# Optimization experiments

Measured on AMD Instinct MI355X. Metric: run time of the kernel, lower is better.

The kernel has to match this reference:

```python
import math
import jax, jax.numpy as jnp
import numpy as np

TEMPERATURE = 1.0
TARGET_VARIANCE = 2.0


def _l2_normalize(x, eps=1e-12):
    # matches F.normalize(dim=-1): x / max(||x||_2, eps)
    n = jnp.linalg.norm(x, axis=-1, keepdims=True)
    return x / jnp.maximum(n, eps)


def setup_inputs() -> dict:
    key = jax.random.key(0)
    k1, k2, k3 = jax.random.split(key, 3)
    B, L, D = 16, 2048, 512
    embs = jax.random.normal(k1, (B, L, D), dtype=jnp.float32)
    clip_embs = jax.random.normal(k2, (B, L, D), dtype=jnp.float32)
    mask = jax.random.randint(k3, (B, L), 0, 2, dtype=jnp.int32)
    return {"embs": embs, "clip_embs": clip_embs, "mask": mask}


def reference(embs, clip_embs, mask):
    B, L, D = embs.shape
    p = _l2_normalize(embs)
    q = _l2_normalize(clip_embs)

    # m_b = number of valid tokens per sample; original slices the first m rows
    m = jnp.sum(mask > 0, axis=-1)                      # [B]
    valid = jnp.arange(L)[None, :] < m[:, None]         # [B, L]
    colm = valid[:, None, :]                            # [B, 1, L] column mask

    # batched p @ q^T over the full padded length, masked afterwards
    logits = jnp.einsum('bid,bjd->bij', p, q) / TEMPERATURE  # [B, L, L]
    neg = jnp.finfo(logits.dtype).min
    logp = jax.nn.log_softmax(jnp.where(colm, logits, neg), axis=-1)

    # Gaussian distance weights: base_weight[i, j] = |i - j|
    idx = jnp.arange(L)
    dist = jnp.abs(idx[:, None] - idx[None, :]).astype(embs.dtype)  # [L, L]
    t_un = jnp.exp(-(dist ** 2) / (2.0 * TARGET_VARIANCE ** 2)) / TARGET_VARIANCE * math.sqrt(math.pi * 2.0)
    target = jax.nn.softmax(jnp.where(colm, t_un[None], neg), axis=-1)  # [B, L, L]

    # KL(target || softmax(logits)) = target * (log target - logp), summed over cols
    safe_t = jnp.where(colm, target, 1.0)
    kl = jnp.where(colm, target * (jnp.log(safe_t) - logp), 0.0)
    row_sum = jnp.sum(kl, axis=-1)                      # [B, L]

    # mean over the m valid rows, then mean over batch
    per_sample = jnp.sum(jnp.where(valid, row_sum, 0.0), axis=-1) / m.astype(embs.dtype)
    return jnp.sum(per_sample) / B
```

## Files before the change

kernel.cpp:

```cpp
#include <hip/hip_runtime.h>
#include <hip/hip_bf16.h>

#define BB 16
#define LL 2048
#define DD 512
#define BL (BB*LL)
#define RADIUS 15
#define CF 1.25331414f
#define NSL 6
#define NII 16

typedef __attribute__((ext_vector_type(8))) short short8_t;
typedef __attribute__((ext_vector_type(4))) float f32x4;

static __device__ __forceinline__ unsigned short f2bf(float x){
  unsigned int u = __float_as_uint(x);
  return (unsigned short)((u + 0x7fffu + ((u >> 16) & 1u)) >> 16);
}

static __device__ __forceinline__ void gld_lds16(const void* g, void* l){
  __builtin_amdgcn_global_load_lds(
      (const __attribute__((address_space(1))) unsigned int*)g,
      (__attribute__((address_space(3))) unsigned int*)l, 16, 0, 0);
}

#if __has_builtin(__builtin_amdgcn_cvt_pk_fp8_f32)
static __device__ __forceinline__ long f2fp8x8(float4 x0, float4 x1){
  int w0 = __builtin_amdgcn_cvt_pk_fp8_f32(x0.x, x0.y, 0, false);
  w0     = __builtin_amdgcn_cvt_pk_fp8_f32(x0.z, x0.w, w0, true);
  int w1 = __builtin_amdgcn_cvt_pk_fp8_f32(x1.x, x1.y, 0, false);
  w1     = __builtin_amdgcn_cvt_pk_fp8_f32(x1.z, x1.w, w1, true);
  return ((long)(unsigned)w1 << 32) | (unsigned)w0;
}
#else
static __device__ __forceinline__ unsigned f2fp8_1(float xf){
  unsigned x = __float_as_uint(xf);
  unsigned s = (x >> 24) & 0x80u;
  unsigned ax = x & 0x7fffffffu;
  if (ax >= 0x43e80000u) return s | 0x7eu;
  if (ax <  0x3a800000u) return s;
  unsigned exp = ax >> 23;
  if (exp <= 120){
    unsigned man = (ax & 0x7fffffu) | 0x800000u;
    int rsh = 141 - (int)exp;
    unsigned keep = man >> rsh;
    unsigned rem  = man & ((1u << rsh) - 1u);
    unsigned half = 1u << (rsh - 1);
    keep += (rem > half || (rem == half && (keep & 1u)));
    return s | keep;
  }
  unsigned keep = ax >> 20;
  unsigned rem  = ax & 0xfffffu;
  keep += (rem > 0x80000u || (rem == 0x80000u && (keep & 1u)));
  int code = (int)keep - (120 << 3);
  if (code >= 0x7f) code = 0x7e;
  return s | (unsigned)code;
}
static __device__ __forceinline__ long f2fp8x8(float4 x0, float4 x1){
  unsigned long o = 0;
  o |= (unsigned long)f2fp8_1(x0.x);
  o |= (unsigned long)f2fp8_1(x0.y) << 8;
  o |= (unsigned long)f2fp8_1(x0.z) << 16;
  o |= (unsigned long)f2fp8_1(x0.w) << 24;
  o |= (unsigned long)f2fp8_1(x1.x) << 32;
  o |= (unsigned long)f2fp8_1(x1.y) << 40;
  o |= (unsigned long)f2fp8_1(x1.z) << 48;
  o |= (unsigned long)f2fp8_1(x1.w) << 56;
  return (long)o;
}
#endif


__global__ void mcount_kernel(const int* __restrict__ mask, int* __restrict__ mout){
  int b = blockIdx.x;
  int s = 0;
  for (int j = threadIdx.x; j < LL; j += 256) s += (mask[(size_t)b*LL + j] > 0) ? 1 : 0;
  __shared__ int sred[256];
  sred[threadIdx.x] = s; __syncthreads();
  for (int k = 128; k; k >>= 1){
    if (threadIdx.x < k) sred[threadIdx.x] += sred[threadIdx.x + k];
    __syncthreads();
  }
  if (threadIdx.x == 0) mout[b] = sred[0];
}

__global__ __launch_bounds__(256) void precvt(const float* __restrict__ embs,
                                              const float* __restrict__ clip,
                                              const int* __restrict__ mcnt,
                                              unsigned char* __restrict__ p8,
                                              unsigned char* __restrict__ q8){
  const int lane = threadIdx.x & 63;
  for (int gw = blockIdx.x * 4 + (threadIdx.x >> 6); gw < 2 * BL; gw += 4096 * 4){
    const float* src; unsigned char* dst; int r, b;
    if (gw < BL){ b = gw >> 11; r = gw & 2047; src = embs + (size_t)gw * DD;
                  dst = p8 + (size_t)b * LL * DD; }
    else { int g = gw - BL; b = g >> 11; r = g & 2047; src = clip + (size_t)g * DD;
           dst = q8 + (size_t)b * LL * DD; }
    const int RND = (mcnt[b] + 127) & ~127;
    if (r >= RND) continue;
    float4 x0 = *(const float4*)(src + lane * 8);
    float4 x1 = *(const float4*)(src + lane * 8 + 4);
    float ss = x0.x*x0.x + x0.y*x0.y + x0.z*x0.z + x0.w*x0.w
             + x1.x*x1.x + x1.y*x1.y + x1.z*x1.z + x1.w*x1.w;
    #pragma unroll
    for (int m = 1; m < 64; m <<= 1) ss += __shfl_xor(ss, m, 64);
    float s = 1.0f / fmaxf(sqrtf(ss), 1e-12f);
    float4 y0 = make_float4(x0.x*s, x0.y*s, x0.z*s, x0.w*s);
    float4 y1 = make_float4(x1.x*s, x1.y*s, x1.z*s, x1.w*s);
    long o = f2fp8x8(y0, y1);
    const int kswz = (lane & 3) ^ ((r >> 2) & 3);
    *(long*)(dst + ((size_t)((lane >> 2) * LL + r) << 5) + (kswz << 3)) = o;
  }
}

__global__ __launch_bounds__(256, 4) void gram8(
    const unsigned char* __restrict__ p8, const unsigned char* __restrict__ q8,
    const int* __restrict__ mcnt, float* __restrict__ part )
{
  const int bid = blockIdx.x;
  const int xcd = bid & 7;
  const int b   = (xcd << 1) | ((bid >> 3) & 1);
  const int ii  = (bid >> 4) & (NII - 1);
  const int js  = bid >> 8;
  const int M   = mcnt[b];
  const int nIt = (M + 127) >> 7;
  if (ii >= nIt) return;

  __shared__ alignas(16) unsigned char bsm[3][8192];
  __shared__ float gt[RADIUS + 1];

  const int tid  = threadIdx.x;
  const int wave = tid >> 6;
  const int lane = tid & 63;
  const int col  = lane & 15;
  const int kg   = lane >> 4;
  const int kswz = (kg ^ (col >> 2)) << 3;

  if (tid <= RADIUS)
    gt[tid] = expm1f(CF * __expf(-(float)(tid * tid) * 0.125f));
  __syncthreads();

  const unsigned char* pb = p8 + (size_t)b * LL * DD;
  const unsigned char* qb = q8 + (size_t)b * LL * DD;
  const int njt = (M + 15) >> 4;
  const int S   = (njt > js) ? ((njt - js + NSL - 1) / NSL) : 0;
  if (S == 0) return;

  #define STAGE(BF, JT) do {                                                     \
    const int _j0 = (JT) << 4;                                                   \
    _Pragma("unroll")                                                            \
    for (int u = 0; u < 2; ++u){                                                 \
      const int _kb0 = (wave << 1) + (u << 3);                                   \
      gld_lds16(qb + ((size_t)((_kb0 + (lane >> 5)) * LL + _j0) << 5)            \
                   + ((lane & 31) << 4),                                         \
                (void*)&bsm[BF][_kb0 << 9]);                                     \
    }                                                                            \
  } while (0)

  const int iw = (ii << 7) + (wave << 5);

  long a0[16], a1[16];
  #pragma unroll
  for (int kb = 0; kb < 16; ++kb){
    a0[kb] = *(const long*)(pb + ((size_t)(kb * LL + iw      + col) << 5) + kswz);
    a1[kb] = *(const long*)(pb + ((size_t)(kb * LL + iw + 16 + col) << 5) + kswz);
  }
  #pragma unroll
  for (int kb = 0; kb < 16; ++kb){
    asm volatile("" : "+v"(a0[kb]));
    asm volatile("" : "+v"(a1[kb]));
  }

  float es0[4]={0,0,0,0}, ls0[4]={0,0,0,0}, bg0[4]={0,0,0,0};
  float es1[4]={0,0,0,0}, ls1[4]={0,0,0,0}, bg1[4]={0,0,0,0};

  STAGE(0, js);
  if (S > 1) STAGE(1, js + NSL);

  for (int s = 0; s < S; ++s){
    if (s + 1 < S) { asm volatile("s_waitcnt vmcnt(2)" ::: "memory"); }
    else           { asm volatile("s_waitcnt vmcnt(0)" ::: "memory"); }
    __builtin_amdgcn_s_barrier();
    __builtin_amdgcn_sched_barrier(0);
    if (s + 2 < S) STAGE((s + 2) % 3, js + NSL * (s + 2));

    const int j0 = (js + NSL * s) << 4;
    f32x4 c0 = {0.f,0.f,0.f,0.f}, c1 = {0.f,0.f,0.f,0.f};
    const unsigned char* lb = &bsm[s % 3][(col << 5) + kswz];
    #pragma unroll
    for (int kb = 0; kb < 16; ++kb){
      long bf8 = *(const long*)(lb + (kb << 9));
      c0 = __builtin_amdgcn_mfma_f32_16x16x32_fp8_fp8(a0[kb], bf8, c0, 0, 0, 0);
      c1 = __builtin_amdgcn_mfma_f32_16x16x32_fp8_fp8(a1[kb], bf8, c1, 0, 0, 0);
    }
    const int j = j0 + col;
    if (j < M){
      const int dt0 = j - iw - (kg << 2);
      #pragma unroll
      for (int r = 0; r < 4; ++r){
        float lg = c0[r];
        es0[r] += __expf(lg); ls0[r] += lg;
        int d = dt0 - r; int ad = d < 0 ? -d : d;
        if (ad <= RADIUS) bg0[r] += gt[ad] * lg;
        float lh = c1[r];
        es1[r] += __expf(lh); ls1[r] += lh;
        int d1 = dt0 - 16 - r; int ad1 = d1 < 0 ? -d1 : d1;
        if (ad1 <= RADIUS) bg1[r] += gt[ad1] * lh;
      }
    }
  }
  #undef STAGE

  #pragma unroll
  for (int m = 1; m < 16; m <<= 1){
    #pragma unroll
    for (int r = 0; r < 4; ++r){
      es0[r] += __shfl_xor(es0[r], m, 64); es1[r] += __shfl_xor(es1[r], m, 64);
      ls0[r] += __shfl_xor(ls0[r], m, 64); ls1[r] += __shfl_xor(ls1[r], m, 64);
      bg0[r] += __shfl_xor(bg0[r], m, 64); bg1[r] += __shfl_xor(bg1[r], m, 64);
    }
  }
  if (col == 0){
    #pragma unroll
    for (int r = 0; r < 4; ++r){
      int ia = iw + (kg << 2) + r;
      *(float4*)&part[(((size_t)b * LL + ia) * NSL + js) * 4] = make_float4(es0[r], ls0[r], bg0[r], 0.f);
      int ib = ia + 16;
      *(float4*)&part[(((size_t)b * LL + ib) * NSL + js) * 4] = make_float4(es1[r], ls1[r], bg1[r], 0.f);
    }
  }
}

__global__ __launch_bounds__(256) void finalize1(const float* __restrict__ part,
                                                 const int* __restrict__ mcnt,
                                                 float* __restrict__ psum){
  const int b = blockIdx.x;
  const int M = mcnt[b];
  __shared__ float e1s[16], tts[16], S1[16], TT[16], red[256];
  const int tid = threadIdx.x;
  if (tid < 16){
    float u  = CF * __expf(-(float)(tid * tid) * 0.125f);
    float eu = __expf(u);
    e1s[tid] = eu - 1.0f;
    tts[tid] = u * eu;
  }
  __syncthreads();
  if (tid == 0){
    float a = 0.f, c = 0.f;
    S1[0] = 0.f; TT[0] = 0.f;
    for (int d = 1; d <= RADIUS; ++d){ a += e1s[d]; c += tts[d]; S1[d] = a; TT[d] = c; }
  }
  __syncthreads();
  const float e10 = e1s[0], tt0 = tts[0];
  float acc = 0.f;
  for (int i = tid; i < M; i += 256){
    float es = 0.f, ls = 0.f, bg = 0.f;
    #pragma unroll
    for (int h = 0; h < NSL; ++h){
      float4 v = *(const float4*)&part[(((size_t)b * LL + i) * NSL + h) * 4];
      es += v.x; ls += v.y; bg += v.z;
    }
    int rl = i < RADIUS ? i : RADIUS;
    int rr = (M - 1 - i) < RADIUS ? (M - 1 - i) : RADIUS;
    float Zt = (float)M + e10 + S1[rl] + S1[rr];
    float U  = tt0 + TT[rl] + TT[rr];
    acc += (U - ls - bg) / Zt + logf(es) - logf(Zt);
  }
  red[tid] = acc; __syncthreads();
  for (int k = 128; k; k >>= 1){
    if (tid < k) red[tid] += red[tid + k];
    __syncthreads();
  }
  if (tid == 0) psum[b] = red[0] / (float)M;
}

__global__ void finalize2(const float* __restrict__ psum, float* __restrict__ out){
  if (threadIdx.x == 0){
    float a = 0.f;
    for (int b = 0; b < BB; ++b) a += psum[b];
    out[0] = a / (float)BB;
  }
}

#define TI 32
#define TJ 32
#define LSTR 520

__global__ void fb_qnorm(const float* __restrict__ clip, float* __restrict__ invq){
  int row = blockIdx.x;
  const float* p = clip + (size_t)row * DD;
  float4 v = *(const float4*)(p + (threadIdx.x << 2));
  float ss = v.x*v.x + v.y*v.y + v.z*v.z + v.w*v.w;
  for (int m = 32; m; m >>= 1) ss += __shfl_down(ss, m, 64);
  __shared__ float red[2];
  if ((threadIdx.x & 63) == 0) red[threadIdx.x >> 6] = ss;
  __syncthreads();
  if (threadIdx.x == 0)
    invq[row] = 1.0f / fmaxf(sqrtf(red[0] + red[1]), 1e-12f);
}

__global__ __launch_bounds__(256) void fb_main(
    const float* __restrict__ embs, const float* __restrict__ clip,
    const float* __restrict__ invq, const int* __restrict__ mcnt,
    float* __restrict__ row_sums)
{
  const int b  = blockIdx.y;
  const int M  = mcnt[b];
  const int i0 = blockIdx.x * TI;
  if (i0 >= M) return;
  __shared__ alignas(16) unsigned short qlds[TJ * LSTR];
  __shared__ float gtab[RADIUS + 1];
  __shared__ float partials[2][TI][3];
  const int tid  = threadIdx.x;
  const int wave = tid >> 6;
  const int lane = tid & 63;
  const int col  = lane & 15;
  const int kg   = lane >> 4;
  const int isub = wave >> 1;
  const int jsub = wave & 1;
  const int iw   = i0 + isub * 16;
  if (tid <= RADIUS)
    gtab[tid] = expm1f(CF * expf(-(float)(tid * tid) * 0.125f));
  const int arow = iw + col;
  const float* prow = embs + ((size_t)b * LL + arow) * DD;
  float ss = 0.f;
  for (int kb = 0; kb < 16; ++kb){
    float4 x0 = *(const float4*)(prow + kb * 32 + kg * 8);
    float4 x1 = *(const float4*)(prow + kb * 32 + kg * 8 + 4);
    ss += x0.x*x0.x + x0.y*x0.y + x0.z*x0.z + x0.w*x0.w
        + x1.x*x1.x + x1.y*x1.y + x1.z*x1.z + x1.w*x1.w;
  }
  ss += __shfl_xor(ss, 16, 64);
  ss += __shfl_xor(ss, 32, 64);
  const float sp = 1.0f / fmaxf(sqrtf(ss), 1e-12f);
  short8_t afrag[16];
  for (int kb = 0; kb < 16; ++kb){
    float4 x0 = *(const float4*)(prow + kb * 32 + kg * 8);
    float4 x1 = *(const float4*)(prow + kb * 32 + kg * 8 + 4);
    short8_t f;
    f[0]=(short)f2bf(x0.x*sp); f[1]=(short)f2bf(x0.y*sp);
    f[2]=(short)f2bf(x0.z*sp); f[3]=(short)f2bf(x0.w*sp);
    f[4]=(short)f2bf(x1.x*sp); f[5]=(short)f2bf(x1.y*sp);
    f[6]=(short)f2bf(x1.z*sp); f[7]=(short)f2bf(x1.w*sp);
    afrag[kb] = f;
  }
  float es[4]={0,0,0,0}, lsm[4]={0,0,0,0}, bg[4]={0,0,0,0};
  const int nj = (M + TJ - 1) / TJ;
  for (int jt = 0; jt < nj; ++jt){
    const int jb = jt * TJ;
    __syncthreads();
    {
      const float* qbase = clip + ((size_t)b * LL + jb) * DD;
      for (int u = 0; u < 16; ++u){
        int f  = u * 256 + tid;
        int r  = f >> 7, c4 = f & 127;
        int j  = jb + r;
        ushort4 wv = make_ushort4(0,0,0,0);
        if (j < M){
          float s = invq[b * LL + j];
          float4 x = *(const float4*)(qbase + ((size_t)r << 9) + (c4 << 2));
          wv = make_ushort4(f2bf(x.x*s), f2bf(x.y*s), f2bf(x.z*s), f2bf(x.w*s));
        }
        *reinterpret_cast<ushort4*>(&qlds[r * LSTR + (c4 << 2)]) = wv;
      }
    }
    __syncthreads();
    const int j0 = jb + jsub * 16;
    f32x4 acc = {0.f,0.f,0.f,0.f};
    const unsigned short* bbase = &qlds[(jsub * 16 + col) * LSTR + kg * 8];
    #pragma unroll
    for (int kb = 0; kb < 16; ++kb){
      short8_t bfrag = *reinterpret_cast<const short8_t*>(bbase + kb * 32);
      acc = __builtin_amdgcn_mfma_f32_16x16x32_bf16(afrag[kb], bfrag, acc, 0, 0, 0);
    }
    const int j = j0 + col;
    if (j < M){
      const int dt = j - iw - kg * 4;
      #pragma unroll
      for (int r = 0; r < 4; ++r){
        float lg = acc[r];
        es[r]  += expf(lg);
        lsm[r] += lg;
        int d = dt - r; int ad = d < 0 ? -d : d;
        if (ad <= RADIUS) bg[r] += gtab[ad] * lg;
      }
    }
  }
  #pragma unroll
  for (int m = 1; m < 16; m <<= 1){
    #pragma unroll
    for (int r = 0; r < 4; ++r){
      es[r]  += __shfl_xor(es[r],  m, 64);
      lsm[r] += __shfl_xor(lsm[r], m, 64);
      bg[r]  += __shfl_xor(bg[r],  m, 64);
    }
  }
  if (col == 0){
    #pragma unroll
    for (int r = 0; r < 4; ++r){
      int lrow = isub * 16 + kg * 4 + r;
      partials[jsub][lrow][0] = es[r];
      partials[jsub][lrow][1] = lsm[r];
      partials[jsub][lrow][2] = bg[r];
    }
  }
  __syncthreads();
  if (tid < TI){
    int i = i0 + tid;
    if (i < M){
      float esf = partials[0][tid][0] + partials[1][tid][0];
      float lsf = partials[0][tid][1] + partials[1][tid][1];
      float bgf = partials[0][tid][2] + partials[1][tid][2];
      int dlo = (-RADIUS < -i) ? -i : -RADIUS;
      int dhi = (RADIUS > M - 1 - i) ? (M - 1 - i) : RADIUS;
      float Zt = (float)M, U = 0.f;
      for (int d = dlo; d <= dhi; ++d){
        float uu = CF * expf(-(float)(d * d) * 0.125f);
        float eu = expf(uu);
        Zt += eu - 1.0f;
        U  += uu * eu;
      }
      row_sums[(size_t)b * LL + i] = (U - lsf - bgf) / Zt + logf(esf / Zt);
    }
  }
}

__global__ void fb_finalize(const float* __restrict__ row_sums,
                            const int* __restrict__ mcnt, float* __restrict__ out){
  __shared__ float red[256];
  float acc = 0.f;
  for (int b = 0; b < BB; ++b){
    int M = mcnt[b];
    float s = 0.f;
    for (int i = threadIdx.x; i < M; i += 256) s += row_sums[(size_t)b * LL + i];
    red[threadIdx.x] = s; __syncthreads();
    for (int k = 128; k; k >>= 1){
      if (threadIdx.x < k) red[threadIdx.x] += red[threadIdx.x + k];
      __syncthreads();
    }
    if (threadIdx.x == 0) acc += red[0] / (float)M;
    __syncthreads();
  }
  if (threadIdx.x == 0) out[0] = acc / (float)BB;
}


extern "C" void kernel_launch(void* const* d_in, const int* in_sizes, int n_in,
                              void* d_out, int out_size, void* d_ws, size_t ws_size,
                              hipStream_t stream) {
  const float* embs = (const float*)d_in[0];
  const float* clip = (const float*)d_in[1];
  const int*   mask = (const int*)d_in[2];
  float* out = (float*)d_out;

  const size_t REQ = (size_t)2 * BL * DD
                   + (size_t)BB * LL * NSL * 4 * sizeof(float)
                   + 64 * sizeof(float);
  if (ws_size >= REQ){
    unsigned char* p8 = (unsigned char*)d_ws;
    unsigned char* q8 = p8 + (size_t)BL * DD;
    float* part = (float*)(q8 + (size_t)BL * DD);
    float* psum = part + (size_t)BB * LL * NSL * 4;
    int*   mcnt = (int*)(psum + 16);

    mcount_kernel<<<dim3(BB), 256, 0, stream>>>(mask, mcnt);
    precvt<<<dim3(4096), 256, 0, stream>>>(embs, clip, mcnt, p8, q8);
    gram8<<<dim3(16 * NSL * NII), 256, 0, stream>>>(p8, q8, mcnt, part);
    finalize1<<<dim3(BB), 256, 0, stream>>>(part, mcnt, psum);
    finalize2<<<1, 64, 0, stream>>>(psum, out);
  } else {
    float* ws   = (float*)d_ws;
    float* invq = ws;
    int*   mcnt = (int*)(ws + BL);
    float* rows = ws + BL + 16;
    fb_qnorm<<<dim3(BL), 128, 0, stream>>>(clip, invq);
    mcount_kernel<<<dim3(BB), 256, 0, stream>>>(mask, mcnt);
    fb_main<<<dim3(LL / TI, BB), 256, 0, stream>>>(embs, clip, invq, mcnt, rows);
    fb_finalize<<<1, 256, 0, stream>>>(rows, mcnt, out);
  }
}
```

Measured before the change: 54.14 us.

## Restructure fp8 precvt to 16 lanes per row and tighten q rounding

The precvt kernel now gives each 16-lane group one row, with each lane loading 32 floats as eight float4s. It writes the swizzled fp8 output as two 16-byte stores instead of one 8-byte store, and the grid-stride loop is replaced by one row group per wavefront quarter. q rows are now converted only up to M rounded to 16 rather than 128, which skips more unused rows. This relies on gram8 never reading q columns past that bound. The MFMA loop in gram8 is also wrapped with s_setprio to favour matrix issue.

After: 55.65 us. 1.03x slower.

```diff
diff --git a/kernel.cpp b/kernel.cpp
--- a/kernel.cpp
+++ b/kernel.cpp
@@ -12,6 +12,7 @@
 
 typedef __attribute__((ext_vector_type(8))) short short8_t;
 typedef __attribute__((ext_vector_type(4))) float f32x4;
+typedef __attribute__((ext_vector_type(2))) long long2_t;
 
 static __device__ __forceinline__ unsigned short f2bf(float x){
   unsigned int u = __float_as_uint(x);
@@ -90,27 +91,49 @@
                                               unsigned char* __restrict__ p8,
                                               unsigned char* __restrict__ q8){
   const int lane = threadIdx.x & 63;
-  for (int gw = blockIdx.x * 4 + (threadIdx.x >> 6); gw < 2 * BL; gw += 4096 * 4){
-    const float* src; unsigned char* dst; int r, b;
-    if (gw < BL){ b = gw >> 11; r = gw & 2047; src = embs + (size_t)gw * DD;
-                  dst = p8 + (size_t)b * LL * DD; }
-    else { int g = gw - BL; b = g >> 11; r = g & 2047; src = clip + (size_t)g * DD;
-           dst = q8 + (size_t)b * LL * DD; }
-    const int RND = (mcnt[b] + 127) & ~127;
-    if (r >= RND) continue;
-    float4 x0 = *(const float4*)(src + lane * 8);
-    float4 x1 = *(const float4*)(src + lane * 8 + 4);
-    float ss = x0.x*x0.x + x0.y*x0.y + x0.z*x0.z + x0.w*x0.w
-             + x1.x*x1.x + x1.y*x1.y + x1.z*x1.z + x1.w*x1.w;
-    #pragma unroll
-    for (int m = 1; m < 64; m <<= 1) ss += __shfl_xor(ss, m, 64);
-    float s = 1.0f / fmaxf(sqrtf(ss), 1e-12f);
-    float4 y0 = make_float4(x0.x*s, x0.y*s, x0.z*s, x0.w*s);
-    float4 y1 = make_float4(x1.x*s, x1.y*s, x1.z*s, x1.w*s);
-    long o = f2fp8x8(y0, y1);
-    const int kswz = (lane & 3) ^ ((r >> 2) & 3);
-    *(long*)(dst + ((size_t)((lane >> 2) * LL + r) << 5) + (kswz << 3)) = o;
-  }
+  const int g    = lane >> 4;
+  const int c    = lane & 15;
+  const int base = blockIdx.x * 16 + (threadIdx.x >> 6) * 4;
+  const int gw   = base + g;
+
+  const float* src; unsigned char* dst; int r, b; bool isP;
+  if (gw < BL){ isP = true;  b = gw >> 11; r = gw & 2047;
+                src = embs + (size_t)gw * DD; dst = p8 + (size_t)b * LL * DD; }
+  else        { isP = false; int g2 = gw - BL; b = g2 >> 11; r = g2 & 2047;
+                src = clip + (size_t)g2 * DD; dst = q8 + (size_t)b * LL * DD; }
+  const int M   = mcnt[b];
+  const int RND = isP ? ((M + 127) & ~127) : ((M + 15) & ~15);
+  if (r >= RND) return;
+
+  float4 v[8];
+  #pragma unroll
+  for (int k = 0; k < 8; ++k) v[k] = *(const float4*)(src + c * 32 + k * 4);
+  float ss = 0.f;
+  #pragma unroll
+  for (int k = 0; k < 8; ++k)
+    ss += v[k].x*v[k].x + v[k].y*v[k].y + v[k].z*v[k].z + v[k].w*v[k].w;
+  #pragma unroll
+  for (int m = 1; m < 16; m <<= 1) ss += __shfl_xor(ss, m, 64);
+  const float s = 1.0f / fmaxf(sqrtf(ss), 1e-12f);
+  #pragma unroll
+  for (int k = 0; k < 8; ++k){
+    v[k].x *= s; v[k].y *= s; v[k].z *= s; v[k].w *= s;
+  }
+  const long o0 = f2fp8x8(v[0], v[1]);
+  const long o1 = f2fp8x8(v[2], v[3]);
+  const long o2 = f2fp8x8(v[4], v[5]);
+  const long o3 = f2fp8x8(v[6], v[7]);
+  const int xr = (r >> 2) & 3;
+  long2_t lo, hi;
+  switch (xr){
+    case 0: lo = (long2_t){o0, o1}; hi = (long2_t){o2, o3}; break;
+    case 1: lo = (long2_t){o1, o0}; hi = (long2_t){o3, o2}; break;
+    case 2: lo = (long2_t){o2, o3}; hi = (long2_t){o0, o1}; break;
+    default:lo = (long2_t){o3, o2}; hi = (long2_t){o1, o0}; break;
+  }
+  unsigned char* wb = dst + ((size_t)(c * LL + r) << 5);
+  *(long2_t*)(wb)      = lo;
+  *(long2_t*)(wb + 16) = hi;
 }
 
 __global__ __launch_bounds__(256, 4) void gram8(
@@ -187,12 +210,14 @@
     const int j0 = (js + NSL * s) << 4;
     f32x4 c0 = {0.f,0.f,0.f,0.f}, c1 = {0.f,0.f,0.f,0.f};
     const unsigned char* lb = &bsm[s % 3][(col << 5) + kswz];
+    __builtin_amdgcn_s_setprio(1);
     #pragma unroll
     for (int kb = 0; kb < 16; ++kb){
       long bf8 = *(const long*)(lb + (kb << 9));
       c0 = __builtin_amdgcn_mfma_f32_16x16x32_fp8_fp8(a0[kb], bf8, c0, 0, 0, 0);
       c1 = __builtin_amdgcn_mfma_f32_16x16x32_fp8_fp8(a1[kb], bf8, c1, 0, 0, 0);
     }
+    __builtin_amdgcn_s_setprio(0);
     const int j = j0 + col;
     if (j < M){
       const int dt0 = j - iw - (kg << 2);
@@ -464,7 +489,7 @@
     int*   mcnt = (int*)(psum + 16);
 
     mcount_kernel<<<dim3(BB), 256, 0, stream>>>(mask, mcnt);
-    precvt<<<dim3(4096), 256, 0, stream>>>(embs, clip, mcnt, p8, q8);
+    precvt<<<dim3(2 * BL / 16), 256, 0, stream>>>(embs, clip, mcnt, p8, q8);
     gram8<<<dim3(16 * NSL * NII), 256, 0, stream>>>(p8, q8, mcnt, part);
     finalize1<<<dim3(BB), 256, 0, stream>>>(part, mcnt, psum);
     finalize2<<<1, 64, 0, stream>>>(psum, out);
```
